# Kernel optimization log

Measured on AMD Instinct MI355X. Metric: run time of the kernel, lower is better.

## Reference

```python
import jax, jax.numpy as jnp
import numpy as np

LAYERS = 5      # lstm_layers
H = 1           # lstm_hidden_size
IN = 21         # 9 (rot) + 6 (v) + 6 (u)
NEG = 0.1       # LeakyReLU negative slope
EPS = 1e-5      # BatchNorm1d eps


def _lstm_cell(x, h, c, w_ih, w_hh):
    # torch gate order: i, f, g, o ; no biases (lstm_bias=False)
    gates = x @ w_ih.T + h @ w_hh.T              # [k, 4H]
    i, f, g, o = jnp.split(gates, 4, axis=-1)
    i = jax.nn.sigmoid(i)
    f = jax.nn.sigmoid(f)
    g = jnp.tanh(g)
    o = jax.nn.sigmoid(o)
    c_new = f * c + i * g
    h_new = o * jnp.tanh(c_new)
    return h_new, c_new


def _bn_train(z, gamma, beta):
    # BatchNorm1d in training mode: batch stats, biased variance
    m = z.mean(axis=0)
    var = z.var(axis=0)
    return gamma * (z - m) / jnp.sqrt(var + EPS) + beta


def setup_inputs() -> dict:
    key = jax.random.key(0)
    ks = jax.random.split(key, 14)
    k, T = 65536, 32
    s = 0.2  # init scale, roughly torch uniform(-1/sqrt(H)) magnitude
    inp = {
        "r": jax.random.normal(ks[0], (k, T, 9), jnp.float32),
        "v": jax.random.normal(ks[1], (k, T, 6), jnp.float32),
        "u": jax.random.normal(ks[2], (k, T, 6), jnp.float32),
        # LSTM weights: layer 0 sees IN features, layers 1..4 see H
        "w_ih0": jax.random.normal(ks[3], (4 * H, IN), jnp.float32) * s,
        "w_ih_rest": jax.random.normal(ks[4], (LAYERS - 1, 4 * H, H), jnp.float32) * s,
        "w_hh": jax.random.normal(ks[5], (LAYERS, 4 * H, H), jnp.float32) * s,
        # FC head: Linear(H,32,no bias) -> BN -> LReLU -> Linear(32,32) -> BN -> LReLU -> Linear(32,6)
        "W1": jax.random.normal(ks[6], (32, H), jnp.float32) * s,
        "g1": jnp.ones((32,), jnp.float32),
        "b1": jnp.zeros((32,), jnp.float32),
        "W2": jax.random.normal(ks[7], (32, 32), jnp.float32) * s,
        "g2": jnp.ones((32,), jnp.float32),
        "b2": jnp.zeros((32,), jnp.float32),
        "W3": jax.random.normal(ks[8], (6, 32), jnp.float32) * s,
    }
    return inp


def reference(r, v, u, w_ih0, w_ih_rest, w_hh, W1, g1, b1, W2, g2, b2, W3):
    x = jnp.concatenate([r, v, u], axis=-1)          # [k, T, 21]
    k = x.shape[0]
    h0 = jnp.zeros((LAYERS, k, H), x.dtype)
    c0 = jnp.zeros((LAYERS, k, H), x.dtype)
    xs = jnp.swapaxes(x, 0, 1)                       # [T, k, 21]

    def step(carry, xt):
        h, c = carry
        hs, cs = [], []
        layer_in = xt
        for l in range(LAYERS):
            w_ih = w_ih0 if l == 0 else w_ih_rest[l - 1]
            hl, cl = _lstm_cell(layer_in, h[l], c[l], w_ih, w_hh[l])
            hs.append(hl)
            cs.append(cl)
            layer_in = hl
        return (jnp.stack(hs), jnp.stack(cs)), layer_in  # top-layer output

    (hT, cT), outs = jax.lax.scan(step, (h0, c0), xs)    # outs: [T, k, H]

    # fc applied to out[:, 0] -> first timestep of top layer
    y = outs[0]                                          # [k, H]
    y = jax.nn.leaky_relu(_bn_train(y @ W1.T, g1, b1), NEG)
    y = jax.nn.leaky_relu(_bn_train(y @ W2.T, g2, b2), NEG)
    dv = y @ W3.T                                        # [k, 6]
    return dv[:, None], hT, cT
```

## Files before the change

kernel.cpp:

```cpp
#include <hip/hip_runtime.h>
#include <math.h>

#define T 32
#define NEGS 0.1f
#define EPS 1e-5f
#define NREG 33


__device__ __forceinline__ float rcp_fast(float x) { return __builtin_amdgcn_rcpf(x); }
__device__ __forceinline__ float sigm(float x) { return rcp_fast(1.0f + __expf(-x)); }
__device__ __forceinline__ float tanh_fast(float x) {
    float t = __expf(2.0f * fabsf(x));
    float r = 1.0f - 2.0f * rcp_fast(t + 1.0f);
    return copysignf(r, x);
}
__device__ __forceinline__ float lrelu(float x) { return x > 0.0f ? x : NEGS * x; }

__device__ __forceinline__ void bn1_params(const float* __restrict__ W1,
                                           const float* __restrict__ g1,
                                           const float* __restrict__ b1,
                                           const double* __restrict__ wsd, int k, int j,
                                           float& my, float& vy, float& a, float& b,
                                           float& tau, int& flip)
{
    my = (float)(wsd[0] / k);
    vy = (float)(wsd[1] / k) - my * my;
    float wj = W1[j];
    a = g1[j] * wj * rsqrtf(fmaf(wj * wj, vy, EPS));
    b = b1[j];
    if (a > 0.0f)      { tau = my - b / a; flip = 0; }
    else if (a < 0.0f) { tau = my - b / a; flip = 1; }
    else               { tau = (b > 0.0f ? -__builtin_inff() : __builtin_inff()); flip = 0; }
}

__global__ __launch_bounds__(256)
void gates_kernel(const float* __restrict__ r, const float* __restrict__ v,
                  const float* __restrict__ u, const float* __restrict__ wih0,
                  float4* __restrict__ xg, int k)
{
    __shared__ float lds[32 * 36];
    const int tid = threadIdx.x;
    const int s0 = blockIdx.x * 8;
    const int sl = tid >> 5, t = tid & 31;
    const size_t st = (size_t)(s0 + sl) * T + t;

    float wi0[4][21];
#pragma unroll
    for (int g = 0; g < 4; ++g)
#pragma unroll
        for (int j = 0; j < 21; ++j) wi0[g][j] = wih0[g * 21 + j];

    const float* rp = r + st * 9;
    const float* vp = v + st * 6;
    const float* up = u + st * 6;
    float x[21];
#pragma unroll
    for (int j = 0; j < 9; ++j) x[j] = rp[j];
#pragma unroll
    for (int j = 0; j < 6; ++j) x[9 + j] = vp[j];
#pragma unroll
    for (int j = 0; j < 6; ++j) x[15 + j] = up[j];

    float4 g4;
    float* gp = (float*)&g4;
#pragma unroll
    for (int g = 0; g < 4; ++g) {
        float acc = 0.f;
#pragma unroll
        for (int j = 0; j < 21; ++j) acc = fmaf(wi0[g][j], x[j], acc);
        gp[g] = acc;
    }
    *(float4*)&lds[t * 36 + sl * 4] = g4;
    __syncthreads();

    const int tG = tid >> 3, j = tid & 7;
    float4 val = *(const float4*)&lds[tG * 36 + j * 4];
    xg[(size_t)tG * k + s0 + j] = val;
}

__global__ __launch_bounds__(256, 1)
void recur_kernel(const float4* __restrict__ xg, const float* __restrict__ wihr,
                  const float* __restrict__ whhp, float* __restrict__ out,
                  double* __restrict__ wsd, float* __restrict__ wsy, int k)
{
    const int s = blockIdx.x * 256 + threadIdx.x;

    float wir[4][4];
#pragma unroll
    for (int l = 0; l < 4; ++l)
#pragma unroll
        for (int g = 0; g < 4; ++g) wir[l][g] = wihr[l * 4 + g];
    float whh[5][4];
#pragma unroll
    for (int l = 0; l < 5; ++l)
#pragma unroll
        for (int g = 0; g < 4; ++g) whh[l][g] = whhp[l * 4 + g];

    float4 gbuf[T];
#pragma unroll
    for (int t = 0; t < T; ++t) gbuf[t] = xg[(size_t)t * k + s];

    float h[5] = {0.f, 0.f, 0.f, 0.f, 0.f};
    float c[5] = {0.f, 0.f, 0.f, 0.f, 0.f};
    float y0 = 0.f;

#pragma unroll
    for (int t = 0; t < T; ++t) {
        const float4 G = gbuf[t];
        float a0 = fmaf(whh[0][0], h[0], G.x);
        float a1 = fmaf(whh[0][1], h[0], G.y);
        float a2 = fmaf(whh[0][2], h[0], G.z);
        float a3 = fmaf(whh[0][3], h[0], G.w);
        {
            float ii = sigm(a0), ff = sigm(a1);
            float gg = tanh_fast(a2), oo = sigm(a3);
            c[0] = ff * c[0] + ii * gg;
            h[0] = oo * tanh_fast(c[0]);
        }
        float xin = h[0];
#pragma unroll
        for (int l = 1; l < 5; ++l) {
            float b0 = fmaf(wir[l - 1][0], xin, whh[l][0] * h[l]);
            float b1 = fmaf(wir[l - 1][1], xin, whh[l][1] * h[l]);
            float b2 = fmaf(wir[l - 1][2], xin, whh[l][2] * h[l]);
            float b3 = fmaf(wir[l - 1][3], xin, whh[l][3] * h[l]);
            float ii = sigm(b0), ff = sigm(b1);
            float gg = tanh_fast(b2), oo = sigm(b3);
            c[l] = ff * c[l] + ii * gg;
            h[l] = oo * tanh_fast(c[l]);
            xin = h[l];
        }
        if (t == 0) y0 = h[4];
    }

#pragma unroll
    for (int l = 0; l < 5; ++l) {
        out[(size_t)6 * k + (size_t)l * k + s] = h[l];
        out[(size_t)11 * k + (size_t)l * k + s] = c[l];
    }
    wsy[s] = y0;

    float ys = y0, yq = y0 * y0;
#pragma unroll
    for (int off = 32; off; off >>= 1) {
        ys += __shfl_down(ys, off);
        yq += __shfl_down(yq, off);
    }
    __shared__ float pS[4], pQ[4];
    const int wid = threadIdx.x >> 6, lane = threadIdx.x & 63;
    if (lane == 0) { pS[wid] = ys; pQ[wid] = yq; }
    __syncthreads();
    if (threadIdx.x == 0) {
        atomicAdd(&wsd[0], (double)(pS[0] + pS[1] + pS[2] + pS[3]));
        atomicAdd(&wsd[1], (double)(pQ[0] + pQ[1] + pQ[2] + pQ[3]));
    }
}

__global__ __launch_bounds__(256, 1)
void lstm_fused(const float* __restrict__ r, const float* __restrict__ v,
                const float* __restrict__ u,
                const float* __restrict__ wih0, const float* __restrict__ wihr,
                const float* __restrict__ whhp,
                float* __restrict__ out, double* __restrict__ wsd,
                float* __restrict__ wsy, int k)
{
    const int s = blockIdx.x * 256 + threadIdx.x;
    float wi0[4][21];
#pragma unroll
    for (int g = 0; g < 4; ++g)
#pragma unroll
        for (int j = 0; j < 21; ++j) wi0[g][j] = wih0[g * 21 + j];
    float wir[4][4];
#pragma unroll
    for (int l = 0; l < 4; ++l)
#pragma unroll
        for (int g = 0; g < 4; ++g) wir[l][g] = wihr[l * 4 + g];
    float whh[5][4];
#pragma unroll
    for (int l = 0; l < 5; ++l)
#pragma unroll
        for (int g = 0; g < 4; ++g) whh[l][g] = whhp[l * 4 + g];

    const float4* r4 = reinterpret_cast<const float4*>(r + (size_t)s * (T * 9));
    const float4* v4 = reinterpret_cast<const float4*>(v + (size_t)s * (T * 6));
    const float4* u4 = reinterpret_cast<const float4*>(u + (size_t)s * (T * 6));

    float h[5] = {0.f, 0.f, 0.f, 0.f, 0.f};
    float c[5] = {0.f, 0.f, 0.f, 0.f, 0.f};
    float y0 = 0.f;

    for (int t0 = 0; t0 < T; t0 += 4) {
        const int cb = t0 >> 2;
        float4 rb[9], vb[6], ub[6];
#pragma unroll
        for (int q = 0; q < 9; ++q) rb[q] = r4[cb * 9 + q];
#pragma unroll
        for (int q = 0; q < 6; ++q) vb[q] = v4[cb * 6 + q];
#pragma unroll
        for (int q = 0; q < 6; ++q) ub[q] = u4[cb * 6 + q];
        float rf[36], vf[24], uf[24];
#pragma unroll
        for (int q = 0; q < 9; ++q) {
            rf[4 * q] = rb[q].x; rf[4 * q + 1] = rb[q].y;
            rf[4 * q + 2] = rb[q].z; rf[4 * q + 3] = rb[q].w;
        }
#pragma unroll
        for (int q = 0; q < 6; ++q) {
            vf[4 * q] = vb[q].x; vf[4 * q + 1] = vb[q].y;
            vf[4 * q + 2] = vb[q].z; vf[4 * q + 3] = vb[q].w;
            uf[4 * q] = ub[q].x; uf[4 * q + 1] = ub[q].y;
            uf[4 * q + 2] = ub[q].z; uf[4 * q + 3] = ub[q].w;
        }
#pragma unroll
        for (int dt = 0; dt < 4; ++dt) {
            float x[21];
#pragma unroll
            for (int j = 0; j < 9; ++j) x[j] = rf[dt * 9 + j];
#pragma unroll
            for (int j = 0; j < 6; ++j) x[9 + j] = vf[dt * 6 + j];
#pragma unroll
            for (int j = 0; j < 6; ++j) x[15 + j] = uf[dt * 6 + j];
            float gt[4];
#pragma unroll
            for (int g = 0; g < 4; ++g) {
                float a = whh[0][g] * h[0];
#pragma unroll
                for (int j = 0; j < 21; ++j) a = fmaf(wi0[g][j], x[j], a);
                gt[g] = a;
            }
            {
                float ii = sigm(gt[0]), ff = sigm(gt[1]);
                float gg = tanh_fast(gt[2]), oo = sigm(gt[3]);
                c[0] = ff * c[0] + ii * gg;
                h[0] = oo * tanh_fast(c[0]);
            }
            float xin = h[0];
#pragma unroll
            for (int l = 1; l < 5; ++l) {
                float b0 = fmaf(wir[l - 1][0], xin, whh[l][0] * h[l]);
                float b1 = fmaf(wir[l - 1][1], xin, whh[l][1] * h[l]);
                float b2 = fmaf(wir[l - 1][2], xin, whh[l][2] * h[l]);
                float b3 = fmaf(wir[l - 1][3], xin, whh[l][3] * h[l]);
                float ii = sigm(b0), ff = sigm(b1);
                float gg = tanh_fast(b2), oo = sigm(b3);
                c[l] = ff * c[l] + ii * gg;
                h[l] = oo * tanh_fast(c[l]);
                xin = h[l];
            }
            if (t0 + dt == 0) y0 = h[4];
        }
    }
#pragma unroll
    for (int l = 0; l < 5; ++l) {
        out[(size_t)6 * k + (size_t)l * k + s] = h[l];
        out[(size_t)11 * k + (size_t)l * k + s] = c[l];
    }
    wsy[s] = y0;
    float ys = y0, yq = y0 * y0;
#pragma unroll
    for (int off = 32; off; off >>= 1) {
        ys += __shfl_down(ys, off);
        yq += __shfl_down(yq, off);
    }
    __shared__ float pS[4], pQ[4];
    const int wid = threadIdx.x >> 6, lane = threadIdx.x & 63;
    if (lane == 0) { pS[wid] = ys; pQ[wid] = yq; }
    __syncthreads();
    if (threadIdx.x == 0) {
        atomicAdd(&wsd[0], (double)(pS[0] + pS[1] + pS[2] + pS[3]));
        atomicAdd(&wsd[1], (double)(pQ[0] + pQ[1] + pQ[2] + pQ[3]));
    }
}

__global__ __launch_bounds__(256)
void hist_kernel(const float* __restrict__ W1, const float* __restrict__ g1,
                 const float* __restrict__ b1, double* __restrict__ wsd,
                 const float* __restrict__ wsy, int k)
{
    __shared__ float sTau[32];
    __shared__ float sH[3 * NREG];
    __shared__ float sMy;
    const int tid = threadIdx.x;
    if (tid < 3 * NREG) sH[tid] = 0.f;
    if (tid < 32) {
        float my, vy, a, b, tau; int flip;
        bn1_params(W1, g1, b1, wsd, k, tid, my, vy, a, b, tau, flip);
        sTau[tid] = tau;
        if (tid == 0) sMy = my;
    }
    __syncthreads();
    const int stride = gridDim.x * 256;
    for (int s = blockIdx.x * 256 + tid; s < k; s += stride) {
        const float y = wsy[s];
        const float yc = y - sMy;
        int rgn = 0;
#pragma unroll
        for (int j = 0; j < 32; ++j) rgn += (y > sTau[j]) ? 1 : 0;
        atomicAdd(&sH[rgn], 1.0f);
        atomicAdd(&sH[NREG + rgn], yc);
        atomicAdd(&sH[2 * NREG + rgn], yc * yc);
    }
    __syncthreads();
    if (tid < 3 * NREG) atomicAdd(&wsd[2 + tid], (double)sH[tid]);
}

__global__ __launch_bounds__(256)
void tables_kernel(const float* __restrict__ W1, const float* __restrict__ g1,
                   const float* __restrict__ b1, const float* __restrict__ W2,
                   const float* __restrict__ g2, const float* __restrict__ b2,
                   const double* __restrict__ wsd, float* __restrict__ gPQ, int k)
{
    __shared__ float sA[32], sB[32], sTau[32];
    __shared__ int sRank[32], sFlip[32];
    __shared__ float sS0[NREG], sS1[NREG], sS2[NREG];
    __shared__ float sW2[1024];
    __shared__ float sSumY1[32];
    __shared__ float sM[1024];
    __shared__ float sI2[32], sM2v[32], sB2[32];
    const int tid = threadIdx.x;

    for (int i = tid; i < 1024; i += 256) sW2[i] = W2[i];
    if (tid < NREG) {
        sS0[tid] = (float)wsd[2 + tid];
        sS1[tid] = (float)wsd[2 + NREG + tid];
        sS2[tid] = (float)wsd[2 + 2 * NREG + tid];
    }
    if (tid < 32) {
        float my, vy, a, b, tau; int flip;
        bn1_params(W1, g1, b1, wsd, k, tid, my, vy, a, b, tau, flip);
        sA[tid] = a; sB[tid] = b; sTau[tid] = tau; sFlip[tid] = flip;
        sB2[tid] = b2[tid];
    }
    __syncthreads();
    if (tid < 32) {
        int rk = 0;
        float tj = sTau[tid];
#pragma unroll
        for (int l = 0; l < 32; ++l)
            rk += (sTau[l] < tj || (sTau[l] == tj && l < tid)) ? 1 : 0;
        sRank[tid] = rk;
    }
    __syncthreads();
    if (tid < 32) {
        const int rk = sRank[tid], fl = sFlip[tid];
        const float a = sA[tid], b = sB[tid];
        float acc = 0.f;
        for (int rg = 0; rg < NREG; ++rg) {
            float m = (((rk < rg) ? 1 : 0) != fl) ? 1.0f : NEGS;
            acc += m * (a * sS1[rg] + b * sS0[rg]);
        }
        sSumY1[tid] = acc;
    }
    for (int p = tid; p < 1024; p += 256) {
        const int j = p >> 5, l = p & 31;
        const int rj = sRank[j], fj = sFlip[j];
        const int rl = sRank[l], flp = sFlip[l];
        const float aj = sA[j], bj = sB[j], al = sA[l], bl = sB[l];
        const float caa = aj * al, cab = aj * bl + al * bj, cbb = bj * bl;
        float acc = 0.f;
        for (int rg = 0; rg < NREG; ++rg) {
            float mj = (((rj < rg) ? 1 : 0) != fj) ? 1.0f : NEGS;
            float ml = (((rl < rg) ? 1 : 0) != flp) ? 1.0f : NEGS;
            acc += mj * ml * (caa * sS2[rg] + cab * sS1[rg] + cbb * sS0[rg]);
        }
        sM[p] = acc;
    }
    __syncthreads();
    if (tid < 32) {
        const int i = tid;
        float s2 = 0.f, ss2 = 0.f;
#pragma unroll
        for (int j = 0; j < 32; ++j) {
            float wij = sW2[i * 32 + j];
            s2 = fmaf(wij, sSumY1[j], s2);
            float tj = 0.f;
#pragma unroll
            for (int l = 0; l < 32; ++l) tj = fmaf(sW2[i * 32 + l], sM[j * 32 + l], tj);
            ss2 = fmaf(wij, tj, ss2);
        }
        float m2 = s2 / k;
        float v2 = ss2 / k - m2 * m2;
        sM2v[i] = m2;
        sI2[i] = g2[i] * rsqrtf(v2 + EPS);
    }
    __syncthreads();
    for (int idx = tid; idx < NREG * 32; idx += 256) {
        const int rg = idx >> 5, i = idx & 31;
        float Ai = 0.f, Bi = 0.f;
#pragma unroll
        for (int j = 0; j < 32; ++j) {
            float m = (((sRank[j] < rg) ? 1 : 0) != sFlip[j]) ? 1.0f : NEGS;
            float w = sW2[i * 32 + j] * m;
            Ai = fmaf(w, sA[j], Ai);
            Bi = fmaf(w, sB[j], Bi);
        }
        gPQ[idx] = sI2[i] * Ai;
        gPQ[NREG * 32 + idx] = sI2[i] * (Bi - sM2v[i]) + sB2[i];
    }
}

__global__ __launch_bounds__(256)
void final_kernel(const float* __restrict__ W1, const float* __restrict__ g1,
                  const float* __restrict__ b1, const float* __restrict__ W3,
                  const double* __restrict__ wsd, const float* __restrict__ wsy,
                  const float* __restrict__ gPQ, float* __restrict__ out, int k)
{
    __shared__ float sTau[32], sW3[192], sMy;
    __shared__ float sP[NREG][33], sQ[NREG][33];
    const int tid = threadIdx.x;
    for (int idx = tid; idx < NREG * 32; idx += 256) {
        const int rg = idx >> 5, i = idx & 31;
        sP[rg][i] = gPQ[idx];
        sQ[rg][i] = gPQ[NREG * 32 + idx];
    }
    if (tid < 192) sW3[tid] = W3[tid];
    if (tid < 32) {
        float my, vy, a, b, tau; int flip;
        bn1_params(W1, g1, b1, wsd, k, tid, my, vy, a, b, tau, flip);
        sTau[tid] = tau;
        if (tid == 0) sMy = my;
    }
    __syncthreads();
    const int s = blockIdx.x * 256 + tid;
    const float y = wsy[s];
    const float yc = y - sMy;
    int rgn = 0;
#pragma unroll
    for (int j = 0; j < 32; ++j) rgn += (y > sTau[j]) ? 1 : 0;
    float dv[6] = {0.f, 0.f, 0.f, 0.f, 0.f, 0.f};
#pragma unroll
    for (int i = 0; i < 32; ++i) {
        float y2 = lrelu(fmaf(sP[rgn][i], yc, sQ[rgn][i]));
#pragma unroll
        for (int m = 0; m < 6; ++m) dv[m] = fmaf(sW3[m * 32 + i], y2, dv[m]);
    }
#pragma unroll
    for (int m = 0; m < 6; ++m) out[(size_t)s * 6 + m] = dv[m];
}

extern "C" void kernel_launch(void* const* d_in, const int* in_sizes, int n_in,
                              void* d_out, int out_size, void* d_ws, size_t ws_size,
                              hipStream_t stream)
{
    const float* r    = (const float*)d_in[0];
    const float* v    = (const float*)d_in[1];
    const float* u    = (const float*)d_in[2];
    const float* wih0 = (const float*)d_in[3];
    const float* wihr = (const float*)d_in[4];
    const float* whhp = (const float*)d_in[5];
    const float* W1   = (const float*)d_in[6];
    const float* g1v  = (const float*)d_in[7];
    const float* b1v  = (const float*)d_in[8];
    const float* W2   = (const float*)d_in[9];
    const float* g2v  = (const float*)d_in[10];
    const float* b2v  = (const float*)d_in[11];
    const float* W3   = (const float*)d_in[12];

    const int k = in_sizes[0] / (T * 9);
    float* out = (float*)d_out;
    double* wsd = (double*)d_ws;
    float* wsy = (float*)((char*)d_ws + 1024);

    const size_t xg_off = 1024 + (size_t)k * 4;
    const size_t need = xg_off + (size_t)k * T * 16 + (size_t)NREG * 32 * 2 * 4;

    hipMemsetAsync(d_ws, 0, 1024, stream);

    const int blocks = k / 256;
    float* gPQ;
    if (ws_size >= need) {
        float4* xg = (float4*)((char*)d_ws + xg_off);
        gPQ = (float*)((char*)d_ws + xg_off + (size_t)k * T * 16);
        gates_kernel<<<k / 8, 256, 0, stream>>>(r, v, u, wih0, xg, k);
        recur_kernel<<<blocks, 256, 0, stream>>>(xg, wihr, whhp, out, wsd, wsy, k);
    } else {
        gPQ = (float*)((char*)d_ws + xg_off);
        lstm_fused<<<blocks, 256, 0, stream>>>(r, v, u, wih0, wihr, whhp, out, wsd, wsy, k);
    }
    hist_kernel<<<64, 256, 0, stream>>>(W1, g1v, b1v, wsd, wsy, k);
    tables_kernel<<<1, 256, 0, stream>>>(W1, g1v, b1v, W2, g2v, b2v, wsd, gPQ, k);
    final_kernel<<<blocks, 256, 0, stream>>>(W1, g1v, b1v, W3, wsd, wsy, gPQ, out, k);
}
```

Measured before the change: 262.0 us.

## Stage gate inputs through LDS and replace global atomics with per-block partials

The gates kernel now loads each block's r/v/u rows into shared memory with coalesced float4 reads instead of strided per-thread scalar loads. The global double atomics for the batch statistics and the histogram are replaced by per-block partial sums, which later kernels reduce, so the workspace memset is no longer needed. Tables now export tau and the mean so the final kernel skips recomputing them. The cost is extra shared memory in the gates kernel and redundant reductions of the partials in the hist and tables kernels.

```diff
diff --git a/kernel.cpp b/kernel.cpp
--- a/kernel.cpp
+++ b/kernel.cpp
@@ -5,6 +5,7 @@
 #define NEGS 0.1f
 #define EPS 1e-5f
 #define NREG 33
+#define NH (3 * NREG)
 
 
 __device__ __forceinline__ float rcp_fast(float x) { return __builtin_amdgcn_rcpf(x); }
@@ -16,15 +17,12 @@
 }
 __device__ __forceinline__ float lrelu(float x) { return x > 0.0f ? x : NEGS * x; }
 
-__device__ __forceinline__ void bn1_params(const float* __restrict__ W1,
-                                           const float* __restrict__ g1,
-                                           const float* __restrict__ b1,
-                                           const double* __restrict__ wsd, int k, int j,
-                                           float& my, float& vy, float& a, float& b,
-                                           float& tau, int& flip)
-{
-    my = (float)(wsd[0] / k);
-    vy = (float)(wsd[1] / k) - my * my;
+__device__ __forceinline__ void bn1_ab(const float* __restrict__ W1,
+                                       const float* __restrict__ g1,
+                                       const float* __restrict__ b1,
+                                       float my, float vy, int j,
+                                       float& a, float& b, float& tau, int& flip)
+{
     float wj = W1[j];
     a = g1[j] * wj * rsqrtf(fmaf(wj * wj, vy, EPS));
     b = b1[j];
@@ -33,16 +31,48 @@
     else               { tau = (b > 0.0f ? -__builtin_inff() : __builtin_inff()); flip = 0; }
 }
 
+__device__ __forceinline__ void reduce_stats(const double* __restrict__ bSums, int nb, int k,
+                                             float* outMy, float* outVy)
+{
+    const int tid = threadIdx.x;
+    double sy = 0.0, sq = 0.0;
+    for (int i = tid; i < nb; i += 256) { sy += bSums[2 * i]; sq += bSums[2 * i + 1]; }
+#pragma unroll
+    for (int off = 32; off; off >>= 1) {
+        sy += __shfl_down(sy, off);
+        sq += __shfl_down(sq, off);
+    }
+    __shared__ double dS[4], dQ[4];
+    const int wid = tid >> 6, lane = tid & 63;
+    if (lane == 0) { dS[wid] = sy; dQ[wid] = sq; }
+    __syncthreads();
+    if (tid == 0) {
+        double tS = dS[0] + dS[1] + dS[2] + dS[3];
+        double tQ = dQ[0] + dQ[1] + dQ[2] + dQ[3];
+        float my = (float)(tS / k);
+        *outMy = my;
+        *outVy = (float)(tQ / k) - my * my;
+    }
+    __syncthreads();
+}
+
 __global__ __launch_bounds__(256)
 void gates_kernel(const float* __restrict__ r, const float* __restrict__ v,
                   const float* __restrict__ u, const float* __restrict__ wih0,
                   float4* __restrict__ xg, int k)
 {
-    __shared__ float lds[32 * 36];
+    __shared__ float rS[2304], vS[1536], uS[1536];
+    __shared__ float gT[32 * 36];
     const int tid = threadIdx.x;
     const int s0 = blockIdx.x * 8;
     const int sl = tid >> 5, t = tid & 31;
-    const size_t st = (size_t)(s0 + sl) * T + t;
+
+    const float4* rG = (const float4*)(r + (size_t)s0 * 288);
+    const float4* vG = (const float4*)(v + (size_t)s0 * 192);
+    const float4* uG = (const float4*)(u + (size_t)s0 * 192);
+    for (int i = tid; i < 576; i += 256) ((float4*)rS)[i] = rG[i];
+    for (int i = tid; i < 384; i += 256) ((float4*)vS)[i] = vG[i];
+    for (int i = tid; i < 384; i += 256) ((float4*)uS)[i] = uG[i];
 
     float wi0[4][21];
 #pragma unroll
@@ -50,16 +80,15 @@
 #pragma unroll
         for (int j = 0; j < 21; ++j) wi0[g][j] = wih0[g * 21 + j];
 
-    const float* rp = r + st * 9;
-    const float* vp = v + st * 6;
-    const float* up = u + st * 6;
+    __syncthreads();
+
     float x[21];
 #pragma unroll
-    for (int j = 0; j < 9; ++j) x[j] = rp[j];
-#pragma unroll
-    for (int j = 0; j < 6; ++j) x[9 + j] = vp[j];
-#pragma unroll
-    for (int j = 0; j < 6; ++j) x[15 + j] = up[j];
+    for (int j = 0; j < 9; ++j) x[j] = rS[sl * 288 + t * 9 + j];
+#pragma unroll
+    for (int j = 0; j < 6; ++j) x[9 + j] = vS[sl * 192 + t * 6 + j];
+#pragma unroll
+    for (int j = 0; j < 6; ++j) x[15 + j] = uS[sl * 192 + t * 6 + j];
 
     float4 g4;
     float* gp = (float*)&g4;
@@ -70,18 +99,18 @@
         for (int j = 0; j < 21; ++j) acc = fmaf(wi0[g][j], x[j], acc);
         gp[g] = acc;
     }
-    *(float4*)&lds[t * 36 + sl * 4] = g4;
+    *(float4*)&gT[t * 36 + sl * 4] = g4;
     __syncthreads();
 
     const int tG = tid >> 3, j = tid & 7;
-    float4 val = *(const float4*)&lds[tG * 36 + j * 4];
+    float4 val = *(const float4*)&gT[tG * 36 + j * 4];
     xg[(size_t)tG * k + s0 + j] = val;
 }
 
 __global__ __launch_bounds__(256, 1)
 void recur_kernel(const float4* __restrict__ xg, const float* __restrict__ wihr,
                   const float* __restrict__ whhp, float* __restrict__ out,
-                  double* __restrict__ wsd, float* __restrict__ wsy, int k)
+                  double* __restrict__ bSums, float* __restrict__ wsy, int k)
 {
     const int s = blockIdx.x * 256 + threadIdx.x;
 
@@ -151,8 +180,8 @@
     if (lane == 0) { pS[wid] = ys; pQ[wid] = yq; }
     __syncthreads();
     if (threadIdx.x == 0) {
-        atomicAdd(&wsd[0], (double)(pS[0] + pS[1] + pS[2] + pS[3]));
-        atomicAdd(&wsd[1], (double)(pQ[0] + pQ[1] + pQ[2] + pQ[3]));
+        bSums[2 * blockIdx.x] = (double)(pS[0] + pS[1] + pS[2] + pS[3]);
+        bSums[2 * blockIdx.x + 1] = (double)(pQ[0] + pQ[1] + pQ[2] + pQ[3]);
     }
 }
 
@@ -161,7 +190,7 @@
                 const float* __restrict__ u,
                 const float* __restrict__ wih0, const float* __restrict__ wihr,
                 const float* __restrict__ whhp,
-                float* __restrict__ out, double* __restrict__ wsd,
+                float* __restrict__ out, double* __restrict__ bSums,
                 float* __restrict__ wsy, int k)
 {
     const int s = blockIdx.x * 256 + threadIdx.x;
@@ -267,32 +296,33 @@
     if (lane == 0) { pS[wid] = ys; pQ[wid] = yq; }
     __syncthreads();
     if (threadIdx.x == 0) {
-        atomicAdd(&wsd[0], (double)(pS[0] + pS[1] + pS[2] + pS[3]));
-        atomicAdd(&wsd[1], (double)(pQ[0] + pQ[1] + pQ[2] + pQ[3]));
+        bSums[2 * blockIdx.x] = (double)(pS[0] + pS[1] + pS[2] + pS[3]);
+        bSums[2 * blockIdx.x + 1] = (double)(pQ[0] + pQ[1] + pQ[2] + pQ[3]);
     }
 }
 
 __global__ __launch_bounds__(256)
 void hist_kernel(const float* __restrict__ W1, const float* __restrict__ g1,
-                 const float* __restrict__ b1, double* __restrict__ wsd,
-                 const float* __restrict__ wsy, int k)
-{
+                 const float* __restrict__ b1, const double* __restrict__ bSums, int nb,
+                 float* __restrict__ bHist, const float* __restrict__ wsy, int k)
+{
+    __shared__ float sMy, sVy;
     __shared__ float sTau[32];
-    __shared__ float sH[3 * NREG];
-    __shared__ float sMy;
+    __shared__ float sH[NH];
     const int tid = threadIdx.x;
-    if (tid < 3 * NREG) sH[tid] = 0.f;
+    reduce_stats(bSums, nb, k, &sMy, &sVy);
+    if (tid < NH) sH[tid] = 0.f;
     if (tid < 32) {
-        float my, vy, a, b, tau; int flip;
-        bn1_params(W1, g1, b1, wsd, k, tid, my, vy, a, b, tau, flip);
+        float a, b, tau; int flip;
+        bn1_ab(W1, g1, b1, sMy, sVy, tid, a, b, tau, flip);
         sTau[tid] = tau;
-        if (tid == 0) sMy = my;
-    }
-    __syncthreads();
+    }
+    __syncthreads();
+    const float my = sMy;
     const int stride = gridDim.x * 256;
     for (int s = blockIdx.x * 256 + tid; s < k; s += stride) {
         const float y = wsy[s];
-        const float yc = y - sMy;
+        const float yc = y - my;
         int rgn = 0;
 #pragma unroll
         for (int j = 0; j < 32; ++j) rgn += (y > sTau[j]) ? 1 : 0;
@@ -301,15 +331,18 @@
         atomicAdd(&sH[2 * NREG + rgn], yc * yc);
     }
     __syncthreads();
-    if (tid < 3 * NREG) atomicAdd(&wsd[2 + tid], (double)sH[tid]);
+    if (tid < NH) bHist[blockIdx.x * NH + tid] = sH[tid];
 }
 
 __global__ __launch_bounds__(256)
 void tables_kernel(const float* __restrict__ W1, const float* __restrict__ g1,
                    const float* __restrict__ b1, const float* __restrict__ W2,
                    const float* __restrict__ g2, const float* __restrict__ b2,
-                   const double* __restrict__ wsd, float* __restrict__ gPQ, int k)
-{
+                   const double* __restrict__ bSums, int nb,
+                   const float* __restrict__ bHist, int nhb,
+                   float* __restrict__ gPQ, int k)
+{
+    __shared__ float sMy, sVy;
     __shared__ float sA[32], sB[32], sTau[32];
     __shared__ int sRank[32], sFlip[32];
     __shared__ float sS0[NREG], sS1[NREG], sS2[NREG];
@@ -319,15 +352,18 @@
     __shared__ float sI2[32], sM2v[32], sB2[32];
     const int tid = threadIdx.x;
 
+    reduce_stats(bSums, nb, k, &sMy, &sVy);
     for (int i = tid; i < 1024; i += 256) sW2[i] = W2[i];
-    if (tid < NREG) {
-        sS0[tid] = (float)wsd[2 + tid];
-        sS1[tid] = (float)wsd[2 + NREG + tid];
-        sS2[tid] = (float)wsd[2 + 2 * NREG + tid];
+    if (tid < NH) {
+        float acc = 0.f;
+        for (int bk = 0; bk < nhb; ++bk) acc += bHist[bk * NH + tid];
+        if (tid < NREG)           sS0[tid] = acc;
+        else if (tid < 2 * NREG)  sS1[tid - NREG] = acc;
+        else                      sS2[tid - 2 * NREG] = acc;
     }
     if (tid < 32) {
-        float my, vy, a, b, tau; int flip;
-        bn1_params(W1, g1, b1, wsd, k, tid, my, vy, a, b, tau, flip);
+        float a, b, tau; int flip;
+        bn1_ab(W1, g1, b1, sMy, sVy, tid, a, b, tau, flip);
         sA[tid] = a; sB[tid] = b; sTau[tid] = tau; sFlip[tid] = flip;
         sB2[tid] = b2[tid];
     }
@@ -397,12 +433,12 @@
         gPQ[idx] = sI2[i] * Ai;
         gPQ[NREG * 32 + idx] = sI2[i] * (Bi - sM2v[i]) + sB2[i];
     }
+    if (tid < 32) gPQ[2 * NREG * 32 + tid] = sTau[tid];
+    if (tid == 0) gPQ[2 * NREG * 32 + 32] = sMy;
 }
 
 __global__ __launch_bounds__(256)
-void final_kernel(const float* __restrict__ W1, const float* __restrict__ g1,
-                  const float* __restrict__ b1, const float* __restrict__ W3,
-                  const double* __restrict__ wsd, const float* __restrict__ wsy,
+void final_kernel(const float* __restrict__ W3, const float* __restrict__ wsy,
                   const float* __restrict__ gPQ, float* __restrict__ out, int k)
 {
     __shared__ float sTau[32], sW3[192], sMy;
@@ -414,12 +450,8 @@
         sQ[rg][i] = gPQ[NREG * 32 + idx];
     }
     if (tid < 192) sW3[tid] = W3[tid];
-    if (tid < 32) {
-        float my, vy, a, b, tau; int flip;
-        bn1_params(W1, g1, b1, wsd, k, tid, my, vy, a, b, tau, flip);
-        sTau[tid] = tau;
-        if (tid == 0) sMy = my;
-    }
+    if (tid < 32) sTau[tid] = gPQ[2 * NREG * 32 + tid];
+    if (tid == 0) sMy = gPQ[2 * NREG * 32 + 32];
     __syncthreads();
     const int s = blockIdx.x * 256 + tid;
     const float y = wsy[s];
@@ -457,27 +489,28 @@
     const float* W3   = (const float*)d_in[12];
 
     const int k = in_sizes[0] / (T * 9);
+    const int blocks = k / 256;
+    const int HB = 64;
     float* out = (float*)d_out;
-    double* wsd = (double*)d_ws;
-    float* wsy = (float*)((char*)d_ws + 1024);
-
-    const size_t xg_off = 1024 + (size_t)k * 4;
-    const size_t need = xg_off + (size_t)k * T * 16 + (size_t)NREG * 32 * 2 * 4;
-
-    hipMemsetAsync(d_ws, 0, 1024, stream);
-
-    const int blocks = k / 256;
+
+    double* bSums = (double*)d_ws;
+    float* bHist  = (float*)((char*)d_ws + 4096);
+    float* wsy    = (float*)((char*)d_ws + 32768);
+    const size_t xg_off = 32768 + (size_t)k * 4;
+    const size_t need = xg_off + (size_t)k * T * 16 + 2176 * 4;
+
     float* gPQ;
     if (ws_size >= need) {
         float4* xg = (float4*)((char*)d_ws + xg_off);
         gPQ = (float*)((char*)d_ws + xg_off + (size_t)k * T * 16);
         gates_kernel<<<k / 8, 256, 0, stream>>>(r, v, u, wih0, xg, k);
-        recur_kernel<<<blocks, 256, 0, stream>>>(xg, wihr, whhp, out, wsd, wsy, k);
+        recur_kernel<<<blocks, 256, 0, stream>>>(xg, wihr, whhp, out, bSums, wsy, k);
     } else {
         gPQ = (float*)((char*)d_ws + xg_off);
-        lstm_fused<<<blocks, 256, 0, stream>>>(r, v, u, wih0, wihr, whhp, out, wsd, wsy, k);
-    }
-    hist_kernel<<<64, 256, 0, stream>>>(W1, g1v, b1v, wsd, wsy, k);
-    tables_kernel<<<1, 256, 0, stream>>>(W1, g1v, b1v, W2, g2v, b2v, wsd, gPQ, k);
-    final_kernel<<<blocks, 256, 0, stream>>>(W1, g1v, b1v, W3, wsd, wsy, gPQ, out, k);
-}
+        lstm_fused<<<blocks, 256, 0, stream>>>(r, v, u, wih0, wihr, whhp, out, bSums, wsy, k);
+    }
+    hist_kernel<<<HB, 256, 0, stream>>>(W1, g1v, b1v, bSums, blocks, bHist, wsy, k);
+    tables_kernel<<<1, 256, 0, stream>>>(W1, g1v, b1v, W2, g2v, b2v, bSums, blocks,
+                                         bHist, HB, gPQ, k);
+    final_kernel<<<blocks, 256, 0, stream>>>(W3, wsy, gPQ, out, k);
+}
```

Result: slower. 270.7 us (+3.3%).
